# Optimization experiments

Hardware: AMD Instinct MI355X
Metric: run time of the kernel (lower is better)

Reference implementation:

```python
import jax, jax.numpy as jnp
import numpy as np

M, C = 262144, 256

def setup_inputs() -> dict:
    key = jax.random.key(0)
    kA, = jax.random.split(key, 1)
    A = jax.random.normal(kA, (M, C), dtype=jnp.float32)
    beta = jnp.zeros((), dtype=jnp.float32)
    return {"A": A, "beta": beta}

def reference(A, beta):
    # interaction: (C, C) = A^T A
    interaction = jnp.einsum('mc,md->cd', A, A)
    CAG = jax.nn.softmax(interaction, axis=-1)  # (C, C), softmax over rows
    # temp = CAG @ A^T -> (C, M); temp^T = A @ CAG^T -> (M, C)
    temp_t = jnp.einsum('md,cd->mc', A, CAG)
    E = A + beta * temp_t
    return (E, CAG)
```

## Files before the change

### kernel.cpp

```cpp
#include <hip/hip_runtime.h>

#define M_ROWS 262144
#define C_DIM 256

#define NBLK 256
#define ROWS_PER_BLK 1024
#define KSTEP 64
#define NSTEP (ROWS_PER_BLK / KSTEP)

typedef __attribute__((ext_vector_type(8))) short short8;
typedef __attribute__((ext_vector_type(16))) float f32x16;

static __device__ __forceinline__ unsigned short f2bf(float x) {
    unsigned int u = __float_as_uint(x);
    u += 0x7FFFu + ((u >> 16) & 1u);
    return (unsigned short)(u >> 16);
}

__global__ __launch_bounds__(1024, 4) void k_pass1(const float* __restrict__ A,
                                                   const float* __restrict__ betap,
                                                   float* __restrict__ E,
                                                   float* __restrict__ part,
                                                   int atomic_mode) {
    __shared__ unsigned short AT[2][C_DIM * KSTEP];

    const int tid = threadIdx.x;
    const int l = tid & 63;
    const int w = tid >> 6;
    const int wr = w >> 2;
    const int wc = w & 3;
    const int lane31 = l & 31;
    const int h = l >> 5;
    const bool copyE = (*betap == 0.0f);
    const size_t mbase = (size_t)blockIdx.x * ROWS_PER_BLK;

    const int c = tid & 255;
    const int mq = tid >> 8;

    f32x16 acc[2][2];
#pragma unroll
    for (int i = 0; i < 2; i++)
#pragma unroll
        for (int j = 0; j < 2; j++)
#pragma unroll
            for (int r = 0; r < 16; r++) acc[i][j][r] = 0.0f;

    auto stage = [&](int s) {
        const size_t m0 = mbase + (size_t)s * KSTEP;
        const float4* A4 = reinterpret_cast<const float4*>(A) + m0 * (C_DIM / 4);
        float4* E4 = reinterpret_cast<float4*>(E) + m0 * (C_DIM / 4);
        if (copyE) {
#pragma unroll
            for (int j = 0; j < 4; j++) E4[j * 1024 + tid] = A4[j * 1024 + tid];
        } else {
#pragma unroll
            for (int j = 0; j < 4; j++) {
                float4 v = A4[j * 1024 + tid];
                asm volatile("" ::"v"(v.x));
            }
        }
        unsigned short* dst = AT[s & 1];
        const float* Ac = A + m0 * C_DIM + c;
#pragma unroll
        for (int j2 = 0; j2 < 2; j2++) {
            const int kb = mq * 16 + j2 * 8;
            unsigned short t0 = f2bf(Ac[(size_t)(kb + 0) * C_DIM]);
            unsigned short t1 = f2bf(Ac[(size_t)(kb + 1) * C_DIM]);
            unsigned short t2 = f2bf(Ac[(size_t)(kb + 2) * C_DIM]);
            unsigned short t3 = f2bf(Ac[(size_t)(kb + 3) * C_DIM]);
            unsigned short t4 = f2bf(Ac[(size_t)(kb + 4) * C_DIM]);
            unsigned short t5 = f2bf(Ac[(size_t)(kb + 5) * C_DIM]);
            unsigned short t6 = f2bf(Ac[(size_t)(kb + 6) * C_DIM]);
            unsigned short t7 = f2bf(Ac[(size_t)(kb + 7) * C_DIM]);
            uint4 v4;
            v4.x = (unsigned)t0 | ((unsigned)t1 << 16);
            v4.y = (unsigned)t2 | ((unsigned)t3 << 16);
            v4.z = (unsigned)t4 | ((unsigned)t5 << 16);
            v4.w = (unsigned)t6 | ((unsigned)t7 << 16);
            const int slot = kb >> 3;
            *reinterpret_cast<uint4*>(&dst[c * KSTEP + ((slot ^ (c & 7)) << 3)]) = v4;
        }
    };

    auto compute = [&](int s) {
        const unsigned short* src = AT[s & 1];
#pragma unroll
        for (int kk = 0; kk < KSTEP; kk += 16) {
            const int slot = (kk >> 3) + h;
            short8 af[2], bf[2];
#pragma unroll
            for (int ti = 0; ti < 2; ti++) {
                const int r = wr * 64 + ti * 32 + lane31;
                af[ti] = *reinterpret_cast<const short8*>(
                    &src[r * KSTEP + ((slot ^ (r & 7)) << 3)]);
            }
#pragma unroll
            for (int tj = 0; tj < 2; tj++) {
                const int cc = wc * 64 + tj * 32 + lane31;
                bf[tj] = *reinterpret_cast<const short8*>(
                    &src[cc * KSTEP + ((slot ^ (cc & 7)) << 3)]);
            }
#pragma unroll
            for (int ti = 0; ti < 2; ti++)
#pragma unroll
                for (int tj = 0; tj < 2; tj++)
                    acc[ti][tj] = __builtin_amdgcn_mfma_f32_32x32x16_bf16(
                        af[ti], bf[tj], acc[ti][tj], 0, 0, 0);
        }
    };

    stage(0);
    __syncthreads();
    for (int s = 0; s < NSTEP; s++) {
        if (s + 1 < NSTEP) stage(s + 1);
        compute(s);
        __syncthreads();
    }

#pragma unroll
    for (int ti = 0; ti < 2; ti++)
#pragma unroll
        for (int tj = 0; tj < 2; tj++)
#pragma unroll
            for (int reg = 0; reg < 16; reg++) {
                const int r = wr * 64 + ti * 32 + (reg & 3) + 8 * (reg >> 2) + 4 * h;
                const int cc = wc * 64 + tj * 32 + lane31;
                const float v = acc[ti][tj][reg];
                if (atomic_mode)
                    atomicAdd(&part[r * C_DIM + cc], v);
                else
                    part[(size_t)blockIdx.x * (C_DIM * C_DIM) + r * C_DIM + cc] = v;
            }
}

__global__ __launch_bounds__(256) void k_softmax(const float* __restrict__ part,
                                                 int P, float* __restrict__ CAG) {
    const int r = blockIdx.x;
    const int cidx = threadIdx.x;
    float s = 0.0f;
    const float* p = part + (size_t)r * C_DIM + cidx;
#pragma unroll 8
    for (int b = 0; b < P; b++) s += p[(size_t)b * (C_DIM * C_DIM)];

    __shared__ float buf[C_DIM];
    buf[cidx] = s;
    __syncthreads();
    for (int off = 128; off; off >>= 1) {
        if (cidx < off) buf[cidx] = fmaxf(buf[cidx], buf[cidx + off]);
        __syncthreads();
    }
    const float mx = buf[0];
    __syncthreads();
    const float e = expf(s - mx);
    buf[cidx] = e;
    __syncthreads();
    for (int off = 128; off; off >>= 1) {
        if (cidx < off) buf[cidx] += buf[cidx + off];
        __syncthreads();
    }
    CAG[(size_t)r * C_DIM + cidx] = e / buf[0];
}

__global__ __launch_bounds__(256) void k_general(const float* __restrict__ A,
                                                 const float* __restrict__ betap,
                                                 const float* __restrict__ CAG,
                                                 float* __restrict__ E) {
    const float beta = *betap;
    if (beta == 0.0f) return;
    const size_t total = (size_t)M_ROWS * C_DIM;
    for (size_t o = (size_t)blockIdx.x * blockDim.x + threadIdx.x; o < total;
         o += (size_t)gridDim.x * blockDim.x) {
        const size_t m = o >> 8;
        const int cc = (int)(o & 255);
        const float* Am = A + m * C_DIM;
        const float* Cg = CAG + (size_t)cc * C_DIM;
        float a2 = 0.0f;
        for (int d = 0; d < C_DIM; d++) a2 += Am[d] * Cg[d];
        E[o] = Am[cc] + beta * a2;
    }
}

extern "C" void kernel_launch(void* const* d_in, const int* in_sizes, int n_in,
                              void* d_out, int out_size, void* d_ws, size_t ws_size,
                              hipStream_t stream) {
    const float* A = (const float*)d_in[0];
    const float* betap = (const float*)d_in[1];
    float* E = (float*)d_out;
    float* CAG = (float*)d_out + (size_t)M_ROWS * C_DIM;
    float* wsf = (float*)d_ws;

    const size_t part_bytes = (size_t)NBLK * C_DIM * C_DIM * sizeof(float);
    const bool partials = (ws_size >= part_bytes);

    if (!partials) {
        hipMemsetAsync(d_ws, 0, (size_t)C_DIM * C_DIM * sizeof(float), stream);
    }
    k_pass1<<<NBLK, 1024, 0, stream>>>(A, betap, E, wsf, partials ? 0 : 1);
    k_softmax<<<C_DIM, C_DIM, 0, stream>>>(wsf, partials ? NBLK : 1, CAG);
    k_general<<<2048, 256, 0, stream>>>(A, betap, CAG, E);
}
```

Baseline: 553.8 us.

## Load A once as float4 with register prefetch and transpose through LDS

```diff
diff --git a/kernel.cpp b/kernel.cpp
--- a/kernel.cpp
+++ b/kernel.cpp
@@ -17,6 +17,10 @@
     return (unsigned short)(u >> 16);
 }
 
+static __device__ __forceinline__ int swzK(int c) {
+    return (c & 7) ^ ((c >> 3) & 3);
+}
+
 __global__ __launch_bounds__(1024, 4) void k_pass1(const float* __restrict__ A,
                                                    const float* __restrict__ betap,
                                                    float* __restrict__ E,
@@ -34,8 +38,7 @@
     const bool copyE = (*betap == 0.0f);
     const size_t mbase = (size_t)blockIdx.x * ROWS_PER_BLK;
 
-    const int c = tid & 255;
-    const int mq = tid >> 8;
+    const int c0 = (tid & 63) * 4;
 
     f32x16 acc[2][2];
 #pragma unroll
@@ -45,44 +48,31 @@
 #pragma unroll
             for (int r = 0; r < 16; r++) acc[i][j][r] = 0.0f;
 
-    auto stage = [&](int s) {
-        const size_t m0 = mbase + (size_t)s * KSTEP;
-        const float4* A4 = reinterpret_cast<const float4*>(A) + m0 * (C_DIM / 4);
-        float4* E4 = reinterpret_cast<float4*>(E) + m0 * (C_DIM / 4);
-        if (copyE) {
+    const float4* A4 = reinterpret_cast<const float4*>(A) + mbase * (C_DIM / 4);
+    float4* E4 = reinterpret_cast<float4*>(E) + mbase * (C_DIM / 4);
+
+    float4 buf[4];
 #pragma unroll
-            for (int j = 0; j < 4; j++) E4[j * 1024 + tid] = A4[j * 1024 + tid];
-        } else {
+    for (int j = 0; j < 4; j++) buf[j] = A4[j * 1024 + tid];
+
+    for (int s = 0; s < NSTEP; s++) {
+        unsigned short* dst = AT[s & 1];
+        const int sbase = s * 4096;
+        const int nbase = sbase + 4096;
 #pragma unroll
-            for (int j = 0; j < 4; j++) {
-                float4 v = A4[j * 1024 + tid];
-                asm volatile("" ::"v"(v.x));
-            }
+        for (int j = 0; j < 4; j++) {
+            const float4 old = buf[j];
+            const int k = j * 16 + w;
+            const int slot = k >> 3;
+            const int kw = k & 7;
+            dst[(c0 + 0) * KSTEP + ((slot ^ swzK(c0 + 0)) << 3) + kw] = f2bf(old.x);
+            dst[(c0 + 1) * KSTEP + ((slot ^ swzK(c0 + 1)) << 3) + kw] = f2bf(old.y);
+            dst[(c0 + 2) * KSTEP + ((slot ^ swzK(c0 + 2)) << 3) + kw] = f2bf(old.z);
+            dst[(c0 + 3) * KSTEP + ((slot ^ swzK(c0 + 3)) << 3) + kw] = f2bf(old.w);
+            if (copyE) E4[sbase + j * 1024 + tid] = old;
+            if (s + 1 < NSTEP) buf[j] = A4[nbase + j * 1024 + tid];
         }
-        unsigned short* dst = AT[s & 1];
-        const float* Ac = A + m0 * C_DIM + c;
-#pragma unroll
-        for (int j2 = 0; j2 < 2; j2++) {
-            const int kb = mq * 16 + j2 * 8;
-            unsigned short t0 = f2bf(Ac[(size_t)(kb + 0) * C_DIM]);
-            unsigned short t1 = f2bf(Ac[(size_t)(kb + 1) * C_DIM]);
-            unsigned short t2 = f2bf(Ac[(size_t)(kb + 2) * C_DIM]);
-            unsigned short t3 = f2bf(Ac[(size_t)(kb + 3) * C_DIM]);
-            unsigned short t4 = f2bf(Ac[(size_t)(kb + 4) * C_DIM]);
-            unsigned short t5 = f2bf(Ac[(size_t)(kb + 5) * C_DIM]);
-            unsigned short t6 = f2bf(Ac[(size_t)(kb + 6) * C_DIM]);
-            unsigned short t7 = f2bf(Ac[(size_t)(kb + 7) * C_DIM]);
-            uint4 v4;
-            v4.x = (unsigned)t0 | ((unsigned)t1 << 16);
-            v4.y = (unsigned)t2 | ((unsigned)t3 << 16);
-            v4.z = (unsigned)t4 | ((unsigned)t5 << 16);
-            v4.w = (unsigned)t6 | ((unsigned)t7 << 16);
-            const int slot = kb >> 3;
-            *reinterpret_cast<uint4*>(&dst[c * KSTEP + ((slot ^ (c & 7)) << 3)]) = v4;
-        }
-    };
-
-    auto compute = [&](int s) {
+        __syncthreads();
         const unsigned short* src = AT[s & 1];
 #pragma unroll
         for (int kk = 0; kk < KSTEP; kk += 16) {
@@ -92,13 +82,13 @@
             for (int ti = 0; ti < 2; ti++) {
                 const int r = wr * 64 + ti * 32 + lane31;
                 af[ti] = *reinterpret_cast<const short8*>(
-                    &src[r * KSTEP + ((slot ^ (r & 7)) << 3)]);
+                    &src[r * KSTEP + ((slot ^ swzK(r)) << 3)]);
             }
 #pragma unroll
             for (int tj = 0; tj < 2; tj++) {
                 const int cc = wc * 64 + tj * 32 + lane31;
                 bf[tj] = *reinterpret_cast<const short8*>(
-                    &src[cc * KSTEP + ((slot ^ (cc & 7)) << 3)]);
+                    &src[cc * KSTEP + ((slot ^ swzK(cc)) << 3)]);
             }
 #pragma unroll
             for (int ti = 0; ti < 2; ti++)
@@ -107,13 +97,6 @@
                     acc[ti][tj] = __builtin_amdgcn_mfma_f32_32x32x16_bf16(
                         af[ti], bf[tj], acc[ti][tj], 0, 0, 0);
         }
-    };
-
-    stage(0);
-    __syncthreads();
-    for (int s = 0; s < NSTEP; s++) {
-        if (s + 1 < NSTEP) stage(s + 1);
-        compute(s);
         __syncthreads();
     }
 
```

Result: faster. 470.1 us (-15.1%).
